# Kernel optimization log

Hardware: AMD Instinct MI355X
Metric: run time of the kernel (lower is better)

The kernel has to match this reference:

```python
import jax, jax.numpy as jnp
import numpy as np

THRESH = 0.9   # config['thresh_cnn']
R = 2          # config['radius'] -> maxpool kernel 2R+1=5, stride 1, padding R


def setup_inputs() -> dict:
    key = jax.random.key(0)
    # [B=1, C=1, D=64, H=512, W=512]
    pred_vol = jax.random.uniform(key, (1, 1, 64, 512, 512), dtype=jnp.float32)
    return {"pred_vol": pred_vol}


def reference(pred_vol):
    # threshold: keep values > thresh, else 0
    pred_thresh = jnp.where(pred_vol > THRESH, pred_vol, 0.0)
    # 3D max-pool, kernel 2R+1, stride 1, padding R (torch pads with -inf for maxpool)
    k = 2 * R + 1
    mp = jax.lax.reduce_window(
        pred_thresh, -jnp.inf, jax.lax.max,
        window_dimensions=(1, 1, k, k, k),
        window_strides=(1, 1, 1, 1, 1),
        padding=[(0, 0), (0, 0), (R, R), (R, R), (R, R)],
    )
    # keep only strict local maxima of the thresholded volume
    conf_vol = jnp.where((mp > 0.0) & (mp == pred_thresh), mp, 0.0)
    return jnp.squeeze(conf_vol)  # [D, H, W] dense peak confidence map
```

## Files before the change

kernel.cpp:

```cpp
#include <hip/hip_runtime.h>
#include <stdint.h>
#include <utility>


#define THRESH 0.9f

constexpr int D = 64, H = 512, W = 512;
constexpr int HW = H * W;
constexpr int TW = 64;
constexpr int TH = 16;
constexpr int DCHUNK = 16;
constexpr int HALO = 2;
constexpr int LROWS = TH + 2 * HALO;
constexpr int RAWQ = TW / 4 + 2;
constexpr int NQ = LROWS * RAWQ;
constexpr int SLOTS = 384;
constexpr int DEPTH = 5;
constexpr int NS = DCHUNK + 2 * HALO;

typedef float floatx4 __attribute__((ext_vector_type(4)));
using gu32p = const __attribute__((address_space(1))) uint32_t*;
using lu32p = __attribute__((address_space(3))) uint32_t*;

__device__ __forceinline__ float4 max4(float4 a, float4 b) {
    return make_float4(fmaxf(a.x, b.x), fmaxf(a.y, b.y),
                       fmaxf(a.z, b.z), fmaxf(a.w, b.w));
}

__device__ __forceinline__ float4 wmax5s(float f2, float f3, float4 b,
                                         float f8, float f9) {
    const float f4 = b.x, f5 = b.y, f6 = b.z, f7 = b.w;
    const float m45 = fmaxf(f4, f5);
    const float m56 = fmaxf(f5, f6);
    const float m345 = fmaxf(f3, m45);
    const float m456 = fmaxf(f4, m56);
    const float m567 = fmaxf(m56, f7);
    const float m678 = fmaxf(fmaxf(f6, f7), f8);
    float4 r;
    r.x = fmaxf(fmaxf(f2, f6), m345);
    r.y = fmaxf(fmaxf(f3, f7), m456);
    r.z = fmaxf(fmaxf(f4, f8), m567);
    r.w = fmaxf(fmaxf(f5, f9), m678);
    return r;
}

template <int N>
__device__ __forceinline__ void cwait() {
    asm volatile("s_waitcnt vmcnt(%0)" :: "n"(N) : "memory");
}

template <typename F, int... I>
__device__ __forceinline__ void static_for_impl(F&& f,
                                                std::integer_sequence<int, I...>) {
    (f(std::integral_constant<int, I>{}), ...);
}
template <int N, typename F>
__device__ __forceinline__ void static_for(F&& f) {
    static_for_impl(static_cast<F&&>(f), std::make_integer_sequence<int, N>{});
}

__global__ __launch_bounds__(256)
__attribute__((amdgpu_num_vgpr(64)))
void peak3d_kernel(const float* __restrict__ in, float* __restrict__ out) {
    __shared__ float4 raw[DEPTH][SLOTS];

    const int tid = threadIdx.y * 16 + threadIdx.x;
    const int wid = tid >> 6;
    const int lane = tid & 63;
    const int tx = tid & 15;
    const int ty = tid >> 4;

    const int w0 = blockIdx.x * TW;
    const int h0 = blockIdx.y * TH;
    const int d0 = blockIdx.z * DCHUNK;

    const bool hasB = (wid < 2);
    const int sA = min(64 * wid + lane, NQ - 1);
    const int sB = min(64 * (4 + wid) + lane, NQ - 1);
    const int rA = sA / RAWQ, cA = sA % RAWQ;
    const int rB = sB / RAWQ, cB = sB % RAWQ;
    const int ghA = min(max(h0 + rA - HALO, 0), H - 1);
    const int gwA = min(max(w0 + 4 * cA - 4, 0), W - 4);
    const int ghB = min(max(h0 + rB - HALO, 0), H - 1);
    const int gwB = min(max(w0 + 4 * cB - 4, 0), W - 4);
    const int offA = ghA * W + gwA;
    const int offB = ghB * W + gwB;

    const int rbase = ty * RAWQ + tx + 1;
    const bool isL = (tx == 0), isR = (tx == 15);
    const bool edgeW = (isL && w0 == 0) || (isR && w0 == W - TW);
    const int hbase = (ty * RAWQ + (isL ? 0 : RAWQ - 1)) * 2 + (isL ? 1 : 0);

    const float4 zero4 = make_float4(0.f, 0.f, 0.f, 0.f);
    float4 win[5];
    float4 cen[2];
#pragma unroll
    for (int k = 0; k < 5; ++k) win[k] = zero4;
    cen[0] = zero4; cen[1] = zero4;

    auto stage = [&](int t) {
        const int dd = min(max(d0 - HALO + t, 0), D - 1);
        const float* sp = in + dd * HW;
        float4* ldsb = &raw[t % DEPTH][0];
        __builtin_amdgcn_global_load_lds((gu32p)(sp + offA),
                                         (lu32p)(ldsb + 64 * wid), 16, 0, 0);
        if (hasB)
            __builtin_amdgcn_global_load_lds((gu32p)(sp + offB),
                                             (lu32p)(ldsb + 64 * (4 + wid)),
                                             16, 0, 0);
    };

    stage(0); stage(1); stage(2);

    static_for<NS>([&](auto tc) {
        constexpr int t = decltype(tc)::value;

        if (t + 3 < NS) stage(t + 3);

        constexpr int la = (t + 3 <= NS - 1) ? 3 : (NS - 1 - t);
        constexpr int lo = (t - 3 > 4) ? (t - 3) : 4;
        constexpr int sa = (t - 1 >= lo) ? (t - 1 - lo + 1) : 0;
        if (hasB) cwait<2 * la + sa>(); else cwait<la + sa>();
        asm volatile("s_barrier" ::: "memory");

        const float4* bp = &raw[t % DEPTH][0];
        const float4 r0q = bp[rbase + 0 * RAWQ];
        const float4 r1q = bp[rbase + 1 * RAWQ];
        const float4 r2q = bp[rbase + 2 * RAWQ];
        const float4 r3q = bp[rbase + 3 * RAWQ];
        const float4 r4q = bp[rbase + 4 * RAWQ];
        const float4 hv = max4(max4(max4(r0q, r1q), max4(r3q, r4q)), r2q);

        float2 h = make_float2(0.f, 0.f);
        if (isL || isR) {
            const float2* hp = reinterpret_cast<const float2*>(bp);
            const float2 e0 = hp[hbase + 0 * RAWQ * 2];
            const float2 e1 = hp[hbase + 1 * RAWQ * 2];
            const float2 e2 = hp[hbase + 2 * RAWQ * 2];
            const float2 e3 = hp[hbase + 3 * RAWQ * 2];
            const float2 e4 = hp[hbase + 4 * RAWQ * 2];
            h.x = fmaxf(fmaxf(fmaxf(e0.x, e1.x), fmaxf(e3.x, e4.x)), e2.x);
            h.y = fmaxf(fmaxf(fmaxf(e0.y, e1.y), fmaxf(e3.y, e4.y)), e2.y);
            if (edgeW) { h.x = 0.f; h.y = 0.f; }
        }

        float f2 = __shfl_up(hv.z, 1);
        float f3 = __shfl_up(hv.w, 1);
        float f8 = __shfl_down(hv.x, 1);
        float f9 = __shfl_down(hv.y, 1);
        if (isL) { f2 = h.x; f3 = h.y; }
        if (isR) { f8 = h.x; f9 = h.y; }

        win[t % 5] = wmax5s(f2, f3, hv, f8, f9);

        if (t >= 4) {
            const int dout = d0 + (t - 4);
            const float4 mp = max4(max4(max4(win[0], win[1]),
                                        max4(win[2], win[3])), win[4]);
            const float4 c = cen[t & 1];
            floatx4 res;
            res.x = (c.x > THRESH && mp.x == c.x) ? c.x : 0.f;
            res.y = (c.y > THRESH && mp.y == c.y) ? c.y : 0.f;
            res.z = (c.z > THRESH && mp.z == c.z) ? c.z : 0.f;
            res.w = (c.w > THRESH && mp.w == c.w) ? c.w : 0.f;
            floatx4* op = reinterpret_cast<floatx4*>(
                out + (size_t)(dout * HW + (h0 + ty) * W + (w0 + 4 * tx)));
            __builtin_nontemporal_store(res, op);
        }
        cen[t & 1] = r2q;
    });
}

extern "C" void kernel_launch(void* const* d_in, const int* in_sizes, int n_in,
                              void* d_out, int out_size, void* d_ws, size_t ws_size,
                              hipStream_t stream) {
    const float* in = (const float*)d_in[0];
    float* out = (float*)d_out;
    dim3 grid(W / TW, H / TH, D / DCHUNK);
    dim3 block(16, 16, 1);
    hipLaunchKernelGGL(peak3d_kernel, grid, block, 0, stream, in, out);
}
```

Before: 118.4 us.

## Double tile height so each thread computes two row outputs per depth slice

Tile height grows from 16 to 32 rows, so each thread now processes two output rows (ty and ty+16), each with its own sliding depth window. Each tile's 4-row H halo is then shared over more outputs, cutting redundant global loads and barriers per output. Staging now issues up to three async global-to-LDS loads per thread per slice, and the vmcnt wait counts are adjusted to match. The VGPR cap of 64 is removed to fit the doubled register state, which raises LDS use per block and may lower occupancy.

```diff
diff --git a/kernel.cpp b/kernel.cpp
--- a/kernel.cpp
+++ b/kernel.cpp
@@ -8,13 +8,13 @@
 constexpr int D = 64, H = 512, W = 512;
 constexpr int HW = H * W;
 constexpr int TW = 64;
-constexpr int TH = 16;
+constexpr int TH = 32;
 constexpr int DCHUNK = 16;
 constexpr int HALO = 2;
 constexpr int LROWS = TH + 2 * HALO;
 constexpr int RAWQ = TW / 4 + 2;
 constexpr int NQ = LROWS * RAWQ;
-constexpr int SLOTS = 384;
+constexpr int SLOTS = 704;
 constexpr int DEPTH = 5;
 constexpr int NS = DCHUNK + 2 * HALO;
 
@@ -60,13 +60,11 @@
 }
 
 __global__ __launch_bounds__(256)
-__attribute__((amdgpu_num_vgpr(64)))
 void peak3d_kernel(const float* __restrict__ in, float* __restrict__ out) {
     __shared__ float4 raw[DEPTH][SLOTS];
 
     const int tid = threadIdx.y * 16 + threadIdx.x;
     const int wid = tid >> 6;
-    const int lane = tid & 63;
     const int tx = tid & 15;
     const int ty = tid >> 4;
 
@@ -74,56 +72,51 @@
     const int h0 = blockIdx.y * TH;
     const int d0 = blockIdx.z * DCHUNK;
 
-    const bool hasB = (wid < 2);
-    const int sA = min(64 * wid + lane, NQ - 1);
-    const int sB = min(64 * (4 + wid) + lane, NQ - 1);
-    const int rA = sA / RAWQ, cA = sA % RAWQ;
-    const int rB = sB / RAWQ, cB = sB % RAWQ;
-    const int ghA = min(max(h0 + rA - HALO, 0), H - 1);
-    const int gwA = min(max(w0 + 4 * cA - 4, 0), W - 4);
-    const int ghB = min(max(h0 + rB - HALO, 0), H - 1);
-    const int gwB = min(max(w0 + 4 * cB - 4, 0), W - 4);
-    const int offA = ghA * W + gwA;
-    const int offB = ghB * W + gwB;
+    const bool hasC = (wid < 3);
+    int offs[3];
+#pragma unroll
+    for (int i = 0; i < 3; ++i) {
+        const int s = min(tid + 256 * i, NQ - 1);
+        const int r = s / RAWQ, c = s % RAWQ;
+        const int gh = min(max(h0 + r - HALO, 0), H - 1);
+        const int gw = min(max(w0 + 4 * c - 4, 0), W - 4);
+        offs[i] = gh * W + gw;
+    }
+    const int off0 = offs[0], off1 = offs[1], off2 = offs[2];
 
-    const int rbase = ty * RAWQ + tx + 1;
     const bool isL = (tx == 0), isR = (tx == 15);
     const bool edgeW = (isL && w0 == 0) || (isR && w0 == W - TW);
-    const int hbase = (ty * RAWQ + (isL ? 0 : RAWQ - 1)) * 2 + (isL ? 1 : 0);
+    const int rbaseA = ty * RAWQ + tx + 1;
+    const int rbaseB = (ty + 16) * RAWQ + tx + 1;
+    const int hcolq = isL ? 0 : (RAWQ - 1);
+    const int hbaseA = (ty * RAWQ + hcolq) * 2 + (isL ? 1 : 0);
+    const int hbaseB = ((ty + 16) * RAWQ + hcolq) * 2 + (isL ? 1 : 0);
 
     const float4 zero4 = make_float4(0.f, 0.f, 0.f, 0.f);
-    float4 win[5];
-    float4 cen[2];
+    float4 winA[5], winB[5];
+    float4 cenA[2], cenB[2];
 #pragma unroll
-    for (int k = 0; k < 5; ++k) win[k] = zero4;
-    cen[0] = zero4; cen[1] = zero4;
+    for (int k = 0; k < 5; ++k) { winA[k] = zero4; winB[k] = zero4; }
+    cenA[0] = zero4; cenA[1] = zero4; cenB[0] = zero4; cenB[1] = zero4;
 
     auto stage = [&](int t) {
         const int dd = min(max(d0 - HALO + t, 0), D - 1);
         const float* sp = in + dd * HW;
         float4* ldsb = &raw[t % DEPTH][0];
-        __builtin_amdgcn_global_load_lds((gu32p)(sp + offA),
+        __builtin_amdgcn_global_load_lds((gu32p)(sp + off0),
                                          (lu32p)(ldsb + 64 * wid), 16, 0, 0);
-        if (hasB)
-            __builtin_amdgcn_global_load_lds((gu32p)(sp + offB),
-                                             (lu32p)(ldsb + 64 * (4 + wid)),
+        __builtin_amdgcn_global_load_lds((gu32p)(sp + off1),
+                                         (lu32p)(ldsb + 256 + 64 * wid), 16, 0, 0);
+        if (hasC)
+            __builtin_amdgcn_global_load_lds((gu32p)(sp + off2),
+                                             (lu32p)(ldsb + 512 + 64 * wid),
                                              16, 0, 0);
     };
 
-    stage(0); stage(1); stage(2);
+    auto consume = [&](const float4* bp, int rbase, int hbase, int hrow,
+                       float4 (&win)[5], float4 (&cen)[2], auto tcc) {
+        constexpr int t = decltype(tcc)::value;
 
-    static_for<NS>([&](auto tc) {
-        constexpr int t = decltype(tc)::value;
-
-        if (t + 3 < NS) stage(t + 3);
-
-        constexpr int la = (t + 3 <= NS - 1) ? 3 : (NS - 1 - t);
-        constexpr int lo = (t - 3 > 4) ? (t - 3) : 4;
-        constexpr int sa = (t - 1 >= lo) ? (t - 1 - lo + 1) : 0;
-        if (hasB) cwait<2 * la + sa>(); else cwait<la + sa>();
-        asm volatile("s_barrier" ::: "memory");
-
-        const float4* bp = &raw[t % DEPTH][0];
         const float4 r0q = bp[rbase + 0 * RAWQ];
         const float4 r1q = bp[rbase + 1 * RAWQ];
         const float4 r2q = bp[rbase + 2 * RAWQ];
@@ -164,10 +157,28 @@
             res.z = (c.z > THRESH && mp.z == c.z) ? c.z : 0.f;
             res.w = (c.w > THRESH && mp.w == c.w) ? c.w : 0.f;
             floatx4* op = reinterpret_cast<floatx4*>(
-                out + (size_t)(dout * HW + (h0 + ty) * W + (w0 + 4 * tx)));
+                out + (size_t)(dout * HW + (h0 + hrow) * W + (w0 + 4 * tx)));
             __builtin_nontemporal_store(res, op);
         }
         cen[t & 1] = r2q;
+    };
+
+    stage(0); stage(1); stage(2);
+
+    static_for<NS>([&](auto tc) {
+        constexpr int t = decltype(tc)::value;
+
+        if (t + 3 < NS) stage(t + 3);
+
+        constexpr int la = (NS - 1 - t < 3) ? (NS - 1 - t) : 3;
+        constexpr int lo = (t - 3 > 4) ? (t - 3) : 4;
+        constexpr int sa = 2 * ((t - 1 >= lo) ? (t - 1 - lo + 1) : 0);
+        if (hasC) cwait<3 * la + sa>(); else cwait<2 * la + sa>();
+        asm volatile("s_barrier" ::: "memory");
+
+        const float4* bp = &raw[t % DEPTH][0];
+        consume(bp, rbaseA, hbaseA, ty,      winA, cenA, tc);
+        consume(bp, rbaseB, hbaseB, ty + 16, winB, cenB, tc);
     });
 }
 
```

New measurement: 120.7 us. Within noise of the previous version (+1.9%).
